# Performance work log

Measured on AMD Instinct MI355X. Metric: run time of the kernel, lower is better.

## Reference

```python
import jax, jax.numpy as jnp
import numpy as np
from jax import lax

D = 1024
DI = 2 * D          # mamba inner dim
NS = 16             # ssm state size
DTR = D // 16       # dt rank = 64
KC = 4              # conv kernel
E = 8               # experts
DFF = 2 * D         # expert hidden
TOPK = 2


def _ln(x, g, b):
    mu = x.mean(-1, keepdims=True)
    var = ((x - mu) ** 2).mean(-1, keepdims=True)
    return (x - mu) * lax.rsqrt(var + 1e-5) * g + b


def _silu(x):
    return x * jax.nn.sigmoid(x)


def setup_inputs() -> dict:
    key = jax.random.key(0)
    ks = jax.random.split(key, 20)
    s = 0.02
    inp = {
        "x": jax.random.normal(ks[0], (2, 2048, D), jnp.float32),
        # layernorms
        "ln_mamba_g": jnp.ones((D,), jnp.float32),
        "ln_mamba_b": jnp.zeros((D,), jnp.float32),
        "ln_moe_g": jnp.ones((D,), jnp.float32),
        "ln_moe_b": jnp.zeros((D,), jnp.float32),
        # mamba params
        "in_proj_w": jax.random.normal(ks[1], (2 * DI, D), jnp.float32) * s,
        "in_proj_b": jnp.zeros((2 * DI,), jnp.float32),
        "conv_w": jax.random.normal(ks[2], (DI, KC), jnp.float32) * s,
        "conv_b": jnp.zeros((DI,), jnp.float32),
        "x_proj_w": jax.random.normal(ks[3], (DTR + 2 * NS, DI), jnp.float32) * s,
        "dt_proj_w": jax.random.normal(ks[4], (DI, DTR), jnp.float32) * s,
        "dt_proj_b": jnp.full((DI,), -4.6, jnp.float32),  # softplus -> small dt
        "A_log": jnp.log(jnp.broadcast_to(jnp.arange(1, NS + 1, dtype=jnp.float32), (DI, NS))),
        "D_skip": jnp.ones((DI,), jnp.float32),
        "out_proj_w": jax.random.normal(ks[5], (D, DI), jnp.float32) * s,
        # moe params
        "router_w": jax.random.normal(ks[6], (E, D), jnp.float32) * s,
        "w1": jax.random.normal(ks[7], (E, DFF, D), jnp.float32) * s,
        "b1": jnp.zeros((E, DFF), jnp.float32),
        "w2": jax.random.normal(ks[8], (E, D, DFF), jnp.float32) * s,
        "b2": jnp.zeros((E, D), jnp.float32),
    }
    return inp


def _mamba(x, in_proj_w, in_proj_b, conv_w, conv_b, x_proj_w,
           dt_proj_w, dt_proj_b, A_log, D_skip, out_proj_w):
    Bz, T, _ = x.shape
    xz = x @ in_proj_w.T + in_proj_b            # [B,T,2*DI]
    xi, z = xz[..., :DI], xz[..., DI:]
    # causal depthwise conv, kernel 4
    xp = jnp.pad(xi, ((0, 0), (KC - 1, 0), (0, 0)))
    xc = conv_b + sum(conv_w[:, k] * xp[:, k:k + T, :] for k in range(KC))
    xc = _silu(xc)                              # [B,T,DI]
    proj = xc @ x_proj_w.T                      # [B,T,DTR+2*NS]
    dt_r = proj[..., :DTR]
    Bm = proj[..., DTR:DTR + NS]                # [B,T,NS]
    Cm = proj[..., DTR + NS:]                   # [B,T,NS]
    dt = jax.nn.softplus(dt_r @ dt_proj_w.T + dt_proj_b)  # [B,T,DI]
    A = -jnp.exp(A_log)                         # [DI,NS]

    def step(h, inp):
        xt, dtt, Bt, Ct = inp                   # [B,DI],[B,DI],[B,NS],[B,NS]
        dA = jnp.exp(dtt[:, :, None] * A)       # [B,DI,NS]
        h = dA * h + (dtt * xt)[:, :, None] * Bt[:, None, :]
        y = jnp.einsum('bdn,bn->bd', h, Ct)
        return h, y

    h0 = jnp.zeros((Bz, DI, NS), x.dtype)
    xs = (xc.transpose(1, 0, 2), dt.transpose(1, 0, 2),
          Bm.transpose(1, 0, 2), Cm.transpose(1, 0, 2))
    _, ys = lax.scan(step, h0, xs)              # [T,B,DI]
    y = ys.transpose(1, 0, 2) + xc * D_skip
    y = y * _silu(z)
    return y @ out_proj_w.T                     # [B,T,D]


def _moe(x, router_w, w1, b1, w2, b2):
    logits = x @ router_w.T                     # [B,T,E]
    probs = jax.nn.softmax(logits, axis=-1)
    topv, topi = lax.top_k(probs, TOPK)
    topv = topv / topv.sum(-1, keepdims=True)
    w = (jax.nn.one_hot(topi, E, dtype=x.dtype) * topv[..., None]).sum(-2)  # [B,T,E]
    out = jnp.zeros_like(x)
    for e in range(E):                          # fixed small expert loop
        h1 = _silu(x @ w1[e].T + b1[e])
        ye = h1 @ w2[e].T + b2[e]
        out = out + w[..., e:e + 1] * ye
    return out, {"router_probs": probs}


def reference(x, ln_mamba_g, ln_mamba_b, ln_moe_g, ln_moe_b,
              in_proj_w, in_proj_b, conv_w, conv_b, x_proj_w,
              dt_proj_w, dt_proj_b, A_log, D_skip, out_proj_w,
              router_w, w1, b1, w2, b2):
    h_norm = _ln(x, ln_mamba_g, ln_mamba_b)
    mamba_out = _mamba(h_norm, in_proj_w, in_proj_b, conv_w, conv_b, x_proj_w,
                       dt_proj_w, dt_proj_b, A_log, D_skip, out_proj_w)
    h = x + mamba_out
    h_moe_in = _ln(h, ln_moe_g, ln_moe_b)
    moe_delta, aux = _moe(h_moe_in, router_w, w1, b1, w2, b2)
    h = h + moe_delta
    return (h, aux["router_probs"])
```

## Files before the change

### kernel.cpp

```cpp
#include <hip/hip_runtime.h>
#include <hip/hip_bf16.h>
#include <math.h>

#define NTOK   4096
#define TSEQ   2048
#define DMODEL 1024
#define DINNER 2048
#define NSTATE 16
#define DTRANK 64
#define NEXP   8
#define DFF    2048
#define NCHUNK 32
#define CLEN   64

typedef __attribute__((ext_vector_type(8))) short short8;
typedef __attribute__((ext_vector_type(4))) float f32x4;

__device__ __forceinline__ float fast_rcp(float x){ return __builtin_amdgcn_rcpf(x); }
__device__ __forceinline__ float siluf(float x){ return x * fast_rcp(1.f + __expf(-x)); }

__device__ __forceinline__ unsigned short f2bf(float x){
  unsigned int u = __float_as_uint(x);
  unsigned int r = (u + 0x7FFFu + ((u >> 16) & 1u)) >> 16;
  return (unsigned short)r;
}

__device__ __forceinline__ void split4(float4 a, unsigned short* hi, unsigned short* lo){
  float av[4] = {a.x, a.y, a.z, a.w};
  #pragma unroll
  for (int j=0;j<4;j++){
    unsigned short hu = f2bf(av[j]);
    float hf = __uint_as_float((unsigned int)hu << 16);
    hi[j] = hu;
    lo[j] = f2bf(av[j] - hf);
  }
}

__global__ void zero_kernel(int* __restrict__ p){ p[threadIdx.x] = 0; }

__global__ __launch_bounds__(256) void split_kernel(
    const float* __restrict__ in, unsigned short* __restrict__ hi,
    unsigned short* __restrict__ lo, int n)
{
  int i = (blockIdx.x*256 + threadIdx.x)*4;
  if (i >= n) return;
  float4 v = *(const float4*)(in + i);
  unsigned short ht[4], lt[4];
  split4(v, ht, lt);
  uint2 hw, lw;
  hw.x = (unsigned)ht[0] | ((unsigned)ht[1]<<16);
  hw.y = (unsigned)ht[2] | ((unsigned)ht[3]<<16);
  lw.x = (unsigned)lt[0] | ((unsigned)lt[1]<<16);
  lw.y = (unsigned)lt[2] | ((unsigned)lt[3]<<16);
  *(uint2*)(hi+i) = hw;
  *(uint2*)(lo+i) = lw;
}

__global__ __launch_bounds__(256) void cvt_bf_kernel(
    const float* __restrict__ in, unsigned short* __restrict__ out, int n)
{
  int i = (blockIdx.x*256 + threadIdx.x)*8;
  if (i >= n) return;
  float4 a = *(const float4*)(in+i);
  float4 b = *(const float4*)(in+i+4);
  short8 v;
  v[0]=(short)f2bf(a.x); v[1]=(short)f2bf(a.y); v[2]=(short)f2bf(a.z); v[3]=(short)f2bf(a.w);
  v[4]=(short)f2bf(b.x); v[5]=(short)f2bf(b.y); v[6]=(short)f2bf(b.z); v[7]=(short)f2bf(b.w);
  *(short8*)(out+i) = v;
}

template<int EPI, int BM, bool PS>
__global__ __launch_bounds__(256) void gemm_big(
    const float* __restrict__ A,
    const unsigned short* __restrict__ Ahi, const unsigned short* __restrict__ Alo, int lda,
    const unsigned short* __restrict__ Whi, const unsigned short* __restrict__ Wlo, int ldw,
    int M, int N, int K,
    const float* __restrict__ bias,
    const float* __restrict__ resid, int ldr,
    float* __restrict__ out, int ldo)
{
  constexpr int RG  = BM/64;
  constexpr int TPR = 256/BM;
  constexpr int EA  = 32/TPR;
  const int tid = threadIdx.x;
  const int m0 = blockIdx.y * BM;
  const int n0 = blockIdx.x * 128;

  __shared__ __align__(16) unsigned short Ahs[BM*40];
  __shared__ __align__(16) unsigned short Als[BM*40];
  __shared__ __align__(16) unsigned short Whs[128*40];
  __shared__ __align__(16) unsigned short Wls[128*40];

  const int arow = tid / TPR;
  const int aseg = (tid % TPR) * EA;
  const int wrow = tid >> 1;
  const int wseg = (tid & 1) * 16;

  const float* Ap = PS ? nullptr : (A + (size_t)(m0 + arow)*lda + aseg);
  const unsigned short* Aph = PS ? (Ahi + (size_t)(m0 + arow)*lda + aseg) : nullptr;
  const unsigned short* Apl = PS ? (Alo + (size_t)(m0 + arow)*lda + aseg) : nullptr;
  const bool wok = (n0 + wrow) < N;
  const unsigned short* Whp = Whi + (size_t)(n0 + wrow)*ldw + wseg;
  const unsigned short* Wlp = Wlo + (size_t)(n0 + wrow)*ldw + wseg;

  const int lane = tid & 63;
  const int wv   = tid >> 6;
  const int qd   = lane >> 4;
  const int mr   = lane & 15;

  f32x4 acc[RG][8];
  #pragma unroll
  for (int rg=0; rg<RG; rg++)
    #pragma unroll
    for (int ct=0; ct<8; ct++) acc[rg][ct] = (f32x4){0.f,0.f,0.f,0.f};

  const unsigned short* ardh = &Ahs[(wv*(16*RG) + mr)*40 + qd*8];
  const unsigned short* ardl = &Als[(wv*(16*RG) + mr)*40 + qd*8];
  const unsigned short* brdh = &Whs[mr*40 + qd*8];
  const unsigned short* brdl = &Wls[mr*40 + qd*8];

  const short8 z8 = {0,0,0,0,0,0,0,0};

  for (int kt = 0; kt < K; kt += 32){
    short8 ah[EA/8], al[EA/8];
    if (PS){
      #pragma unroll
      for (int h=0; h<EA/8; h++){
        ah[h] = *(const short8*)(Aph + kt + h*8);
        al[h] = *(const short8*)(Apl + kt + h*8);
      }
    } else {
      #pragma unroll
      for (int q=0; q<EA/4; q++){
        float4 f = *(const float4*)(Ap + kt + q*4);
        unsigned short ht[4], lt[4];
        split4(f, ht, lt);
        #pragma unroll
        for (int j=0;j<4;j++){
          ah[(q*4+j)/8][(q*4+j)&7] = (short)ht[j];
          al[(q*4+j)/8][(q*4+j)&7] = (short)lt[j];
        }
      }
    }
    short8 wh0 = wok ? *(const short8*)(Whp + kt)     : z8;
    short8 wh1 = wok ? *(const short8*)(Whp + kt + 8) : z8;
    short8 wl0 = wok ? *(const short8*)(Wlp + kt)     : z8;
    short8 wl1 = wok ? *(const short8*)(Wlp + kt + 8) : z8;
    __syncthreads();
    #pragma unroll
    for (int h=0; h<EA/8; h++){
      *(short8*)&Ahs[arow*40 + aseg + h*8] = ah[h];
      *(short8*)&Als[arow*40 + aseg + h*8] = al[h];
    }
    *(short8*)&Whs[wrow*40 + wseg]     = wh0;
    *(short8*)&Whs[wrow*40 + wseg + 8] = wh1;
    *(short8*)&Wls[wrow*40 + wseg]     = wl0;
    *(short8*)&Wls[wrow*40 + wseg + 8] = wl1;
    __syncthreads();
    #pragma unroll
    for (int rg=0; rg<RG; rg++){
      short8 af = *(const short8*)(ardh + rg*16*40);
      short8 alf= *(const short8*)(ardl + rg*16*40);
      #pragma unroll
      for (int ct=0; ct<8; ct++){
        short8 bh = *(const short8*)(brdh + ct*16*40);
        short8 bl = *(const short8*)(brdl + ct*16*40);
        f32x4 t = acc[rg][ct];
        t = __builtin_amdgcn_mfma_f32_16x16x32_bf16(af, bh, t, 0,0,0);
        t = __builtin_amdgcn_mfma_f32_16x16x32_bf16(alf, bh, t, 0,0,0);
        t = __builtin_amdgcn_mfma_f32_16x16x32_bf16(af, bl, t, 0,0,0);
        acc[rg][ct] = t;
      }
    }
  }

  #pragma unroll
  for (int rg=0; rg<RG; rg++){
    #pragma unroll
    for (int ct=0; ct<8; ct++){
      int colg = n0 + ct*16 + mr;
      if (colg >= N) continue;
      float bias_v = (EPI==0 || EPI==2) ? bias[colg] : 0.f;
      #pragma unroll
      for (int r=0;r<4;r++){
        int rowg = m0 + wv*(16*RG) + rg*16 + qd*4 + r;
        float v = acc[rg][ct][r];
        if (EPI == 0){ v += bias_v; }
        else if (EPI == 2){ v += bias_v; v = (v > 20.f) ? v : log1pf(expf(v)); }
        else if (EPI == 3){ v += resid[(size_t)rowg*ldr + colg]; }
        out[(size_t)rowg*ldo + colg] = v;
      }
    }
  }
}

__global__ __launch_bounds__(256) void ln_split_kernel(
    const float* __restrict__ x, const float* __restrict__ g, const float* __restrict__ b,
    unsigned short* __restrict__ hi, unsigned short* __restrict__ lo)
{
  int tok = blockIdx.x;
  int tid = threadIdx.x;
  const float* row = x + (size_t)tok * DMODEL;
  float v[4];
  float s = 0.f, sq = 0.f;
  #pragma unroll
  for (int j=0;j<4;j++){
    v[j] = row[j*256 + tid];
    s += v[j]; sq += v[j]*v[j];
  }
  #pragma unroll
  for (int o=1;o<64;o<<=1){ s += __shfl_xor(s,o,64); sq += __shfl_xor(sq,o,64); }
  __shared__ float ss[4], ssq[4];
  int wid = tid >> 6, lane = tid & 63;
  if (lane == 0){ ss[wid]=s; ssq[wid]=sq; }
  __syncthreads();
  s  = ss[0]+ss[1]+ss[2]+ss[3];
  sq = ssq[0]+ssq[1]+ssq[2]+ssq[3];
  float mu = s * (1.f/DMODEL);
  float var = sq * (1.f/DMODEL) - mu*mu;
  float rs = rsqrtf(var + 1e-5f);
  #pragma unroll
  for (int j=0;j<4;j++){
    int d = j*256 + tid;
    float o = (v[j]-mu)*rs*g[d] + b[d];
    unsigned short hu = f2bf(o);
    float hf = __uint_as_float((unsigned int)hu << 16);
    hi[(size_t)tok*DMODEL + d] = hu;
    lo[(size_t)tok*DMODEL + d] = f2bf(o - hf);
  }
}

__global__ __launch_bounds__(256) void ln2_kernel(
    const float* __restrict__ x, const float* __restrict__ g, const float* __restrict__ b,
    float* __restrict__ out, unsigned short* __restrict__ outb)
{
  int tok = blockIdx.x;
  int tid = threadIdx.x;
  const float* row = x + (size_t)tok * DMODEL;
  float v[4];
  float s = 0.f, sq = 0.f;
  #pragma unroll
  for (int j=0;j<4;j++){
    v[j] = row[j*256 + tid];
    s += v[j]; sq += v[j]*v[j];
  }
  #pragma unroll
  for (int o=1;o<64;o<<=1){ s += __shfl_xor(s,o,64); sq += __shfl_xor(sq,o,64); }
  __shared__ float ss[4], ssq[4];
  int wid = tid >> 6, lane = tid & 63;
  if (lane == 0){ ss[wid]=s; ssq[wid]=sq; }
  __syncthreads();
  s  = ss[0]+ss[1]+ss[2]+ss[3];
  sq = ssq[0]+ssq[1]+ssq[2]+ssq[3];
  float mu = s * (1.f/DMODEL);
  float var = sq * (1.f/DMODEL) - mu*mu;
  float rs = rsqrtf(var + 1e-5f);
  #pragma unroll
  for (int j=0;j<4;j++){
    int d = j*256 + tid;
    float o = (v[j]-mu)*rs*g[d] + b[d];
    out[(size_t)tok*DMODEL + d] = o;
    outb[(size_t)tok*DMODEL + d] = f2bf(o);
  }
}

__global__ __launch_bounds__(256) void conv_kernel(
    const float* __restrict__ xz, const float* __restrict__ cw,
    const float* __restrict__ cb, float* __restrict__ xc)
{
  int i = blockIdx.x*256 + threadIdx.x;
  int tok = i >> 11;
  int ch  = i & 2047;
  int t   = tok & (TSEQ-1);
  int b   = tok >> 11;
  float acc = cb[ch];
  #pragma unroll
  for (int k=0;k<4;k++){
    int tt = t + k - 3;
    if (tt >= 0)
      acc = fmaf(cw[ch*4 + k], xz[(size_t)((b<<11)+tt)*4096 + ch], acc);
  }
  xc[i] = siluf(acc);
}

__global__ __launch_bounds__(256) void scan_partial(
    const float* __restrict__ xz, const float* __restrict__ xc,
    const float* __restrict__ proj, const float* __restrict__ A_log,
    float* __restrict__ P, float* __restrict__ Q)
{
  int tid = threadIdx.x;
  int ch  = blockIdx.x*256 + tid;
  int c   = blockIdx.y;
  int b   = blockIdx.z;
  float A[16];
  #pragma unroll
  for (int n=0;n<16;n++) A[n] = -expf(A_log[ch*NSTATE + n]);
  float h[16];
  #pragma unroll
  for (int n=0;n<16;n++) h[n] = 0.f;
  float sdt = 0.f;
  int tok0 = (b<<11) + c*CLEN;
  float dtv = xz[(size_t)tok0*4096 + ch];
  float xt  = xc[(size_t)tok0*2048 + ch];
  for (int i=0;i<CLEN;i++){
    int tn = tok0 + ((i+1 < CLEN) ? i+1 : i);
    float dtv_n = xz[(size_t)tn*4096 + ch];
    float xt_n  = xc[(size_t)tn*2048 + ch];
    const float4* pB = (const float4*)(proj + (size_t)(tok0+i)*96 + 64);
    float Bv[16];
    *(float4*)&Bv[0]  = pB[0];
    *(float4*)&Bv[4]  = pB[1];
    *(float4*)&Bv[8]  = pB[2];
    *(float4*)&Bv[12] = pB[3];
    float dxt = dtv*xt;
    sdt += dtv;
    #pragma unroll
    for (int n=0;n<16;n++){
      float dA = __expf(dtv*A[n]);
      h[n] = fmaf(dA, h[n], dxt*Bv[n]);
    }
    dtv = dtv_n; xt = xt_n;
  }
  size_t base = ((((size_t)(b*NCHUNK + c))<<11 | ch)<<4);
  #pragma unroll
  for (int n=0;n<16;n++){
    P[base+n] = __expf(A[n]*sdt);
    Q[base+n] = h[n];
  }
}

__global__ __launch_bounds__(256) void scan_combine(
    const float* __restrict__ Q, float* PH)
{
  int g = blockIdx.x*256 + threadIdx.x;
  int n = g & 15, ch = (g>>4) & 2047, b = g>>15;
  float hs = 0.f;
  for (int c=0;c<NCHUNK;c++){
    size_t idx = ((((size_t)(b*NCHUNK + c))<<11 | ch)<<4) | n;
    float pv = PH[idx];
    float qv = Q[idx];
    PH[idx] = hs;
    hs = fmaf(pv, hs, qv);
  }
}

__global__ __launch_bounds__(256) void scan_final(
    const float* __restrict__ xz, float* __restrict__ xc,
    const float* __restrict__ proj, const float* __restrict__ A_log,
    const float* __restrict__ Dskip, const float* __restrict__ Hs)
{
  int tid = threadIdx.x;
  int ch  = blockIdx.x*256 + tid;
  int c   = blockIdx.y;
  int b   = blockIdx.z;
  float A[16];
  #pragma unroll
  for (int n=0;n<16;n++) A[n] = -expf(A_log[ch*NSTATE + n]);
  float Dv = Dskip[ch];
  size_t base = ((((size_t)(b*NCHUNK + c))<<11 | ch)<<4);
  float h[16];
  #pragma unroll
  for (int n=0;n<16;n++) h[n] = Hs[base+n];
  int tok0 = (b<<11) + c*CLEN;
  float dtv = xz[(size_t)tok0*4096 + ch];
  float xt  = xc[(size_t)tok0*2048 + ch];
  float zv  = xz[(size_t)tok0*4096 + 2048 + ch];
  for (int i=0;i<CLEN;i++){
    int tn = tok0 + ((i+1 < CLEN) ? i+1 : i);
    float dtv_n = xz[(size_t)tn*4096 + ch];
    float xt_n  = xc[(size_t)tn*2048 + ch];
    float zv_n  = xz[(size_t)tn*4096 + 2048 + ch];
    const float4* pB = (const float4*)(proj + (size_t)(tok0+i)*96 + 64);
    float Bv[16], Cv[16];
    *(float4*)&Bv[0]  = pB[0];
    *(float4*)&Bv[4]  = pB[1];
    *(float4*)&Bv[8]  = pB[2];
    *(float4*)&Bv[12] = pB[3];
    *(float4*)&Cv[0]  = pB[4];
    *(float4*)&Cv[4]  = pB[5];
    *(float4*)&Cv[8]  = pB[6];
    *(float4*)&Cv[12] = pB[7];
    float dxt = dtv*xt;
    float y = xt*Dv;
    #pragma unroll
    for (int n=0;n<16;n++){
      float dA = __expf(dtv*A[n]);
      h[n] = fmaf(dA, h[n], dxt*Bv[n]);
      y = fmaf(h[n], Cv[n], y);
    }
    xc[(size_t)(tok0+i)*2048 + ch] = y * siluf(zv);
    dtv = dtv_n; xt = xt_n; zv = zv_n;
  }
}

__global__ __launch_bounds__(256) void router_kernel(
    const float* __restrict__ hmoe, const float* __restrict__ rw,
    float* __restrict__ probs_out, int* __restrict__ cnt,
    int* __restrict__ tok_e0, int* __restrict__ tok_e1,
    float* __restrict__ tok_w0, float* __restrict__ tok_w1)
{
  int tok = blockIdx.x;
  int tid = threadIdx.x;
  int e = tid >> 5, l = tid & 31;
  float s = 0.f;
  const float* row = hmoe + (size_t)tok*DMODEL;
  const float* wr  = rw + (size_t)e*DMODEL;
  for (int d=l; d<DMODEL; d+=32) s = fmaf(row[d], wr[d], s);
  #pragma unroll
  for (int o=1;o<32;o<<=1) s += __shfl_xor(s,o,64);
  __shared__ float lg[8];
  if (l==0) lg[e]=s;
  __syncthreads();
  if (tid==0){
    float mx = lg[0];
    for (int k=1;k<8;k++) mx = fmaxf(mx, lg[k]);
    float pe[8]; float den=0.f;
    for (int k=0;k<8;k++){ pe[k]=expf(lg[k]-mx); den+=pe[k]; }
    float inv = 1.f/den;
    for (int k=0;k<8;k++) probs_out[tok*8+k] = pe[k]*inv;
    int i0=0;
    for (int k=1;k<8;k++) if (pe[k] > pe[i0]) i0=k;
    int i1 = (i0==0)?1:0;
    for (int k=0;k<8;k++) if (k!=i0 && pe[k] > pe[i1]) i1=k;
    float v0=pe[i0], v1=pe[i1], sw=v0+v1;
    tok_e0[tok]=i0; tok_e1[tok]=i1;
    tok_w0[tok]=v0/sw; tok_w1[tok]=v1/sw;
    atomicAdd(&cnt[i0],1); atomicAdd(&cnt[i1],1);
  }
}

__global__ void prefix_kernel(const int* cnt, int* off, int* fill){
  if (threadIdx.x==0){
    int s=0;
    for (int e=0;e<NEXP;e++){ off[e]=s; s+=cnt[e]; fill[e]=0; }
  }
}

__global__ __launch_bounds__(256) void fill_kernel(
    const int* tok_e0, const int* tok_e1, const float* tok_w0, const float* tok_w1,
    const int* off, int* fill, int* slot_tok, float* slot_w)
{
  int tok = blockIdx.x*256 + threadIdx.x;
  int e0=tok_e0[tok], e1=tok_e1[tok];
  int p0 = atomicAdd(&fill[e0],1); int s0 = off[e0]+p0;
  slot_tok[s0]=tok; slot_w[s0]=tok_w0[tok];
  int p1 = atomicAdd(&fill[e1],1); int s1 = off[e1]+p1;
  slot_tok[s1]=tok; slot_w[s1]=tok_w1[tok];
}

__global__ __launch_bounds__(256) void moe_gemm1(
    const unsigned short* __restrict__ hnb, const unsigned short* __restrict__ w1b,
    const float* __restrict__ b1,
    const int* __restrict__ cnt, const int* __restrict__ off,
    const int* __restrict__ slot_tok, unsigned short* __restrict__ H1)
{
  int e = blockIdx.z;
  int c = cnt[e];
  int r0 = blockIdx.y*128;
  if (r0 >= c) return;
  int base = off[e];
  int tid = threadIdx.x;
  __shared__ int toks[128];
  if (tid < 128) toks[tid] = (r0 + tid < c) ? slot_tok[base + r0 + tid] : -1;
  __shared__ __align__(16) unsigned short As[128*40];
  __shared__ __align__(16) unsigned short Ws[128*40];
  __syncthreads();

  const int n0   = blockIdx.x*128;
  const int srow = tid >> 1;
  const int sseg = (tid & 1) * 16;
  const int tok  = toks[srow];
  const bool aok = (tok >= 0);
  const unsigned short* Ap = hnb + (size_t)(aok ? tok : 0)*DMODEL + sseg;
  const unsigned short* Wp = w1b + (size_t)e*DFF*DMODEL + (size_t)(n0+srow)*DMODEL + sseg;

  const int lane = tid & 63;
  const int wv   = tid >> 6;
  const int qd   = lane >> 4;
  const int mr   = lane & 15;

  f32x4 acc[2][8];
  #pragma unroll
  for (int rg=0; rg<2; rg++)
    #pragma unroll
    for (int ct=0; ct<8; ct++) acc[rg][ct] = (f32x4){0.f,0.f,0.f,0.f};

  const unsigned short* ard = &As[(wv*32 + mr)*40 + qd*8];
  const unsigned short* brd = &Ws[mr*40 + qd*8];
  const short8 z8 = {0,0,0,0,0,0,0,0};

  for (int kt = 0; kt < DMODEL; kt += 32){
    short8 a0 = aok ? *(const short8*)(Ap + kt)     : z8;
    short8 a1 = aok ? *(const short8*)(Ap + kt + 8) : z8;
    short8 w0 = *(const short8*)(Wp + kt);
    short8 w1v= *(const short8*)(Wp + kt + 8);
    __syncthreads();
    *(short8*)&As[srow*40 + sseg]     = a0;
    *(short8*)&As[srow*40 + sseg + 8] = a1;
    *(short8*)&Ws[srow*40 + sseg]     = w0;
    *(short8*)&Ws[srow*40 + sseg + 8] = w1v;
    __syncthreads();
    #pragma unroll
    for (int rg=0; rg<2; rg++){
      short8 af = *(const short8*)(ard + rg*16*40);
      #pragma unroll
      for (int ct=0; ct<8; ct++){
        short8 bf = *(const short8*)(brd + ct*16*40);
        acc[rg][ct] = __builtin_amdgcn_mfma_f32_16x16x32_bf16(af, bf, acc[rg][ct], 0,0,0);
      }
    }
  }

  #pragma unroll
  for (int rg=0; rg<2; rg++){
    #pragma unroll
    for (int ct=0; ct<8; ct++){
      int colg = n0 + ct*16 + mr;
      float bias = b1[(size_t)e*DFF + colg];
      #pragma unroll
      for (int r=0;r<4;r++){
        int sl = wv*32 + rg*16 + qd*4 + r;
        if (toks[sl] < 0) continue;
        float v = acc[rg][ct][r] + bias;
        H1[(size_t)(base + r0 + sl)*DFF + colg] = f2bf(siluf(v));
      }
    }
  }
}

__global__ __launch_bounds__(256) void moe_gemm2(
    const unsigned short* __restrict__ H1, const unsigned short* __restrict__ w2b,
    const float* __restrict__ b2,
    const int* __restrict__ cnt, const int* __restrict__ off,
    const int* __restrict__ slot_tok, const float* __restrict__ slot_w,
    float* __restrict__ hres)
{
  int e = blockIdx.z;
  int c = cnt[e];
  int r0 = blockIdx.y*128;
  if (r0 >= c) return;
  int base = off[e];
  int tid = threadIdx.x;
  __shared__ int toks[128];
  __shared__ float wts[128];
  if (tid < 128){
    int r = r0 + tid;
    toks[tid] = (r<c) ? slot_tok[base+r] : -1;
    wts[tid]  = (r<c) ? slot_w[base+r] : 0.f;
  }
  __shared__ __align__(16) unsigned short As[128*40];
  __shared__ __align__(16) unsigned short Ws[128*40];
  __syncthreads();

  const int n0   = blockIdx.x*128;
  const int srow = tid >> 1;
  const int sseg = (tid & 1) * 16;
  const bool aok = (toks[srow] >= 0);
  const unsigned short* Ap = H1 + (size_t)(base + r0 + (aok ? srow : 0))*DFF + sseg;
  const unsigned short* Wp = w2b + (size_t)e*DMODEL*DFF + (size_t)(n0+srow)*DFF + sseg;

  const int lane = tid & 63;
  const int wv   = tid >> 6;
  const int qd   = lane >> 4;
  const int mr   = lane & 15;

  f32x4 acc[2][8];
  #pragma unroll
  for (int rg=0; rg<2; rg++)
    #pragma unroll
    for (int ct=0; ct<8; ct++) acc[rg][ct] = (f32x4){0.f,0.f,0.f,0.f};

  const unsigned short* ard = &As[(wv*32 + mr)*40 + qd*8];
  const unsigned short* brd = &Ws[mr*40 + qd*8];
  const short8 z8 = {0,0,0,0,0,0,0,0};

  for (int kt = 0; kt < DFF; kt += 32){
    short8 a0 = aok ? *(const short8*)(Ap + kt)     : z8;
    short8 a1 = aok ? *(const short8*)(Ap + kt + 8) : z8;
    short8 w0 = *(const short8*)(Wp + kt);
    short8 w1v= *(const short8*)(Wp + kt + 8);
    __syncthreads();
    *(short8*)&As[srow*40 + sseg]     = a0;
    *(short8*)&As[srow*40 + sseg + 8] = a1;
    *(short8*)&Ws[srow*40 + sseg]     = w0;
    *(short8*)&Ws[srow*40 + sseg + 8] = w1v;
    __syncthreads();
    #pragma unroll
    for (int rg=0; rg<2; rg++){
      short8 af = *(const short8*)(ard + rg*16*40);
      #pragma unroll
      for (int ct=0; ct<8; ct++){
        short8 bf = *(const short8*)(brd + ct*16*40);
        acc[rg][ct] = __builtin_amdgcn_mfma_f32_16x16x32_bf16(af, bf, acc[rg][ct], 0,0,0);
      }
    }
  }

  #pragma unroll
  for (int rg=0; rg<2; rg++){
    #pragma unroll
    for (int ct=0; ct<8; ct++){
      int colg = n0 + ct*16 + mr;
      float bias = b2[(size_t)e*DMODEL + colg];
      #pragma unroll
      for (int r=0;r<4;r++){
        int sl = wv*32 + rg*16 + qd*4 + r;
        int t = toks[sl];
        if (t < 0) continue;
        float v = acc[rg][ct][r] + bias;
        atomicAdd(&hres[(size_t)t*DMODEL + colg], wts[sl]*v);
      }
    }
  }
}

__global__ __launch_bounds__(256) void final_kernel(const float* __restrict__ hres,
                                                    float* __restrict__ out)
{
  int i = blockIdx.x*256 + threadIdx.x;
  out[i] = hres[i];
}

extern "C" void kernel_launch(void* const* d_in, const int* in_sizes, int n_in,
                              void* d_out, int out_size, void* d_ws, size_t ws_size,
                              hipStream_t stream)
{
  const float* x         = (const float*)d_in[0];
  const float* ln_m_g    = (const float*)d_in[1];
  const float* ln_m_b    = (const float*)d_in[2];
  const float* ln_e_g    = (const float*)d_in[3];
  const float* ln_e_b    = (const float*)d_in[4];
  const float* in_proj_w = (const float*)d_in[5];
  const float* in_proj_b = (const float*)d_in[6];
  const float* conv_w    = (const float*)d_in[7];
  const float* conv_b    = (const float*)d_in[8];
  const float* x_proj_w  = (const float*)d_in[9];
  const float* dt_proj_w = (const float*)d_in[10];
  const float* dt_proj_b = (const float*)d_in[11];
  const float* A_log     = (const float*)d_in[12];
  const float* D_skip    = (const float*)d_in[13];
  const float* out_proj_w= (const float*)d_in[14];
  const float* router_w  = (const float*)d_in[15];
  const float* w1        = (const float*)d_in[16];
  const float* b1        = (const float*)d_in[17];
  const float* w2        = (const float*)d_in[18];
  const float* b2        = (const float*)d_in[19];

  char* ws = (char*)d_ws;
  float* xz   = (float*)(ws + 0);
  float* xc   = (float*)(ws + 67108864ull);
  float* proj = (float*)(ws + 100663296ull);
  char*  misc = ws + 102236160ull;
  float* hres = (float*)(ws + 0);
  unsigned short* H1    = (unsigned short*)(ws + 16777216ull);
  unsigned short* hn_bf = (unsigned short*)(ws + 50331648ull);
  unsigned short* wmoe  = (unsigned short*)(ws + 67108864ull);

  unsigned short* hn_hi = (unsigned short*)d_out;
  unsigned short* hn_lo = hn_hi + 4194304;
  float* hn   = (float*)d_out;
  float* Pbuf = (float*)d_out;
  float* Qbuf = (float*)d_out + (2u<<20);

  unsigned short* Wi_hi = (unsigned short*)(ws + 67108864ull);
  unsigned short* Wi_lo = Wi_hi + 4194304;
  unsigned short* Wo_hi = (unsigned short*)(ws + 33554432ull);
  unsigned short* Wo_lo = Wo_hi + 2097152;
  unsigned short* Wx_hi = (unsigned short*)d_out;
  unsigned short* Wx_lo = Wx_hi + 196608;
  unsigned short* Wd_hi = Wx_lo + 196608;
  unsigned short* Wd_lo = Wd_hi + 131072;

  int*   cnt      = (int*)(misc);
  int*   fill     = (int*)(misc + 64);
  int*   offp     = (int*)(misc + 128);
  int*   tok_e0   = (int*)(misc + 1024);
  int*   tok_e1   = (int*)(misc + 1024 + 16384);
  float* tok_w0   = (float*)(misc + 1024 + 32768);
  float* tok_w1   = (float*)(misc + 1024 + 49152);
  int*   slot_tok = (int*)(misc + 1024 + 65536);
  float* slot_w   = (float*)(misc + 1024 + 98304);
  float* out_h    = (float*)d_out;
  float* probs_out= (float*)d_out + 4194304;

  zero_kernel<<<1, 64, 0, stream>>>(cnt);

  split_kernel<<<4096, 256, 0, stream>>>(in_proj_w, Wi_hi, Wi_lo, 4194304);
  ln_split_kernel<<<NTOK, 256, 0, stream>>>(x, ln_m_g, ln_m_b, hn_hi, hn_lo);
  gemm_big<0,128,true><<<dim3(32, 32), 256, 0, stream>>>(
      nullptr, hn_hi, hn_lo, DMODEL, Wi_hi, Wi_lo, DMODEL, NTOK, 4096, DMODEL,
      in_proj_b, nullptr, 0, xz, 4096);
  split_kernel<<<192, 256, 0, stream>>>(x_proj_w, Wx_hi, Wx_lo, 196608);
  split_kernel<<<128, 256, 0, stream>>>(dt_proj_w, Wd_hi, Wd_lo, 131072);
  conv_kernel<<<NTOK*DINNER/256, 256, 0, stream>>>(xz, conv_w, conv_b, xc);
  gemm_big<1,64,false><<<dim3(1, 64), 256, 0, stream>>>(
      xc, nullptr, nullptr, DINNER, Wx_hi, Wx_lo, DINNER, NTOK, 96, DINNER,
      nullptr, nullptr, 0, proj, 96);
  gemm_big<2,128,false><<<dim3(16, 32), 256, 0, stream>>>(
      proj, nullptr, nullptr, 96, Wd_hi, Wd_lo, DTRANK, NTOK, DINNER, DTRANK,
      dt_proj_b, nullptr, 0, xz, 4096);
  scan_partial<<<dim3(DINNER/256, NCHUNK, 2), 256, 0, stream>>>(
      xz, xc, proj, A_log, Pbuf, Qbuf);
  scan_combine<<<256, 256, 0, stream>>>(Qbuf, Pbuf);
  scan_final<<<dim3(DINNER/256, NCHUNK, 2), 256, 0, stream>>>(
      xz, xc, proj, A_log, D_skip, Pbuf);
  split_kernel<<<2048, 256, 0, stream>>>(out_proj_w, Wo_hi, Wo_lo, 2097152);
  gemm_big<3,128,false><<<dim3(8, 32), 256, 0, stream>>>(
      xc, nullptr, nullptr, DINNER, Wo_hi, Wo_lo, DINNER, NTOK, DMODEL, DINNER,
      nullptr, x, DMODEL, hres, DMODEL);

  ln2_kernel<<<NTOK, 256, 0, stream>>>(hres, ln_e_g, ln_e_b, hn, hn_bf);
  router_kernel<<<NTOK, 256, 0, stream>>>(hn, router_w, probs_out, cnt,
                                          tok_e0, tok_e1, tok_w0, tok_w1);
  prefix_kernel<<<1, 64, 0, stream>>>(cnt, offp, fill);
  fill_kernel<<<NTOK/256, 256, 0, stream>>>(tok_e0, tok_e1, tok_w0, tok_w1,
                                            offp, fill, slot_tok, slot_w);
  cvt_bf_kernel<<<8192, 256, 0, stream>>>(w1, wmoe, NEXP*DFF*DMODEL);
  moe_gemm1<<<dim3(DFF/128, 32, NEXP), 256, 0, stream>>>(
      hn_bf, wmoe, b1, cnt, offp, slot_tok, H1);
  cvt_bf_kernel<<<8192, 256, 0, stream>>>(w2, wmoe, NEXP*DMODEL*DFF);
  moe_gemm2<<<dim3(DMODEL/128, 32, NEXP), 256, 0, stream>>>(
      H1, wmoe, b2, cnt, offp, slot_tok, slot_w, hres);

  final_kernel<<<NTOK*DMODEL/256, 256, 0, stream>>>(hres, out_h);
}
```

Measured before the change: 1.056 ms.

## Add split-K and configurable N-tile to gemm, widen in_proj tile, drop final copy

The generic GEMM gains a templated N-tile width and a split-K mode that writes per-slice partial outputs. The narrow x_proj GEMM (N=96) is split four ways along K and the out_proj GEMM two ways, with small reduction kernels summing the partials (the out_proj one also adds the residual). The in_proj GEMM switches to a 256-wide N tile. The MoE accumulates directly into the output buffer, which removes the final copy kernel. The goal is more parallelism for the small-grid GEMMs and less redundant A-tile traffic, paid for by extra partial-sum memory traffic, extra launches and higher register pressure from the wider tile.

```diff
diff --git a/kernel.cpp b/kernel.cpp
--- a/kernel.cpp
+++ b/kernel.cpp
@@ -69,50 +69,54 @@
   *(short8*)(out+i) = v;
 }
 
-template<int EPI, int BM, bool PS>
+template<int EPI, int BM, bool PS, int CT, bool SK>
 __global__ __launch_bounds__(256) void gemm_big(
     const float* __restrict__ A,
     const unsigned short* __restrict__ Ahi, const unsigned short* __restrict__ Alo, int lda,
     const unsigned short* __restrict__ Whi, const unsigned short* __restrict__ Wlo, int ldw,
     int M, int N, int K,
     const float* __restrict__ bias,
-    const float* __restrict__ resid, int ldr,
     float* __restrict__ out, int ldo)
 {
+  constexpr int BN  = CT*16;
   constexpr int RG  = BM/64;
   constexpr int TPR = 256/BM;
   constexpr int EA  = 32/TPR;
+  constexpr int TPW = 256/BN;
+  constexpr int EW  = 32/TPW;
   const int tid = threadIdx.x;
   const int m0 = blockIdx.y * BM;
-  const int n0 = blockIdx.x * 128;
+  const int n0 = blockIdx.x * BN;
+  const int koff = SK ? blockIdx.z * K : 0;
+  float* outp = out + (SK ? (size_t)blockIdx.z * M * ldo : 0);
 
   __shared__ __align__(16) unsigned short Ahs[BM*40];
   __shared__ __align__(16) unsigned short Als[BM*40];
-  __shared__ __align__(16) unsigned short Whs[128*40];
-  __shared__ __align__(16) unsigned short Wls[128*40];
+  __shared__ __align__(16) unsigned short Whs[BN*40];
+  __shared__ __align__(16) unsigned short Wls[BN*40];
 
   const int arow = tid / TPR;
   const int aseg = (tid % TPR) * EA;
-  const int wrow = tid >> 1;
-  const int wseg = (tid & 1) * 16;
-
-  const float* Ap = PS ? nullptr : (A + (size_t)(m0 + arow)*lda + aseg);
-  const unsigned short* Aph = PS ? (Ahi + (size_t)(m0 + arow)*lda + aseg) : nullptr;
-  const unsigned short* Apl = PS ? (Alo + (size_t)(m0 + arow)*lda + aseg) : nullptr;
+  const int wrow = tid / TPW;
+  const int wseg = (tid % TPW) * EW;
+
+  const float* Ap = PS ? nullptr : (A + (size_t)(m0 + arow)*lda + aseg + koff);
+  const unsigned short* Aph = PS ? (Ahi + (size_t)(m0 + arow)*lda + aseg + koff) : nullptr;
+  const unsigned short* Apl = PS ? (Alo + (size_t)(m0 + arow)*lda + aseg + koff) : nullptr;
   const bool wok = (n0 + wrow) < N;
-  const unsigned short* Whp = Whi + (size_t)(n0 + wrow)*ldw + wseg;
-  const unsigned short* Wlp = Wlo + (size_t)(n0 + wrow)*ldw + wseg;
+  const unsigned short* Whp = Whi + (size_t)(n0 + wrow)*ldw + wseg + koff;
+  const unsigned short* Wlp = Wlo + (size_t)(n0 + wrow)*ldw + wseg + koff;
 
   const int lane = tid & 63;
   const int wv   = tid >> 6;
   const int qd   = lane >> 4;
   const int mr   = lane & 15;
 
-  f32x4 acc[RG][8];
+  f32x4 acc[RG][CT];
   #pragma unroll
   for (int rg=0; rg<RG; rg++)
     #pragma unroll
-    for (int ct=0; ct<8; ct++) acc[rg][ct] = (f32x4){0.f,0.f,0.f,0.f};
+    for (int ct=0; ct<CT; ct++) acc[rg][ct] = (f32x4){0.f,0.f,0.f,0.f};
 
   const unsigned short* ardh = &Ahs[(wv*(16*RG) + mr)*40 + qd*8];
   const unsigned short* ardl = &Als[(wv*(16*RG) + mr)*40 + qd*8];
@@ -142,27 +146,30 @@
         }
       }
     }
-    short8 wh0 = wok ? *(const short8*)(Whp + kt)     : z8;
-    short8 wh1 = wok ? *(const short8*)(Whp + kt + 8) : z8;
-    short8 wl0 = wok ? *(const short8*)(Wlp + kt)     : z8;
-    short8 wl1 = wok ? *(const short8*)(Wlp + kt + 8) : z8;
+    short8 wh[EW/8], wl[EW/8];
+    #pragma unroll
+    for (int h=0; h<EW/8; h++){
+      wh[h] = wok ? *(const short8*)(Whp + kt + h*8) : z8;
+      wl[h] = wok ? *(const short8*)(Wlp + kt + h*8) : z8;
+    }
     __syncthreads();
     #pragma unroll
     for (int h=0; h<EA/8; h++){
       *(short8*)&Ahs[arow*40 + aseg + h*8] = ah[h];
       *(short8*)&Als[arow*40 + aseg + h*8] = al[h];
     }
-    *(short8*)&Whs[wrow*40 + wseg]     = wh0;
-    *(short8*)&Whs[wrow*40 + wseg + 8] = wh1;
-    *(short8*)&Wls[wrow*40 + wseg]     = wl0;
-    *(short8*)&Wls[wrow*40 + wseg + 8] = wl1;
+    #pragma unroll
+    for (int h=0; h<EW/8; h++){
+      *(short8*)&Whs[wrow*40 + wseg + h*8] = wh[h];
+      *(short8*)&Wls[wrow*40 + wseg + h*8] = wl[h];
+    }
     __syncthreads();
     #pragma unroll
     for (int rg=0; rg<RG; rg++){
       short8 af = *(const short8*)(ardh + rg*16*40);
       short8 alf= *(const short8*)(ardl + rg*16*40);
       #pragma unroll
-      for (int ct=0; ct<8; ct++){
+      for (int ct=0; ct<CT; ct++){
         short8 bh = *(const short8*)(brdh + ct*16*40);
         short8 bl = *(const short8*)(brdl + ct*16*40);
         f32x4 t = acc[rg][ct];
@@ -177,7 +184,7 @@
   #pragma unroll
   for (int rg=0; rg<RG; rg++){
     #pragma unroll
-    for (int ct=0; ct<8; ct++){
+    for (int ct=0; ct<CT; ct++){
       int colg = n0 + ct*16 + mr;
       if (colg >= N) continue;
       float bias_v = (EPI==0 || EPI==2) ? bias[colg] : 0.f;
@@ -187,11 +194,41 @@
         float v = acc[rg][ct][r];
         if (EPI == 0){ v += bias_v; }
         else if (EPI == 2){ v += bias_v; v = (v > 20.f) ? v : log1pf(expf(v)); }
-        else if (EPI == 3){ v += resid[(size_t)rowg*ldr + colg]; }
-        out[(size_t)rowg*ldo + colg] = v;
+        outp[(size_t)rowg*ldo + colg] = v;
       }
     }
   }
+}
+
+__global__ __launch_bounds__(256) void reduce4_kernel(
+    const float* __restrict__ pp, float* __restrict__ out, int n)
+{
+  int i = (blockIdx.x*256 + threadIdx.x)*4;
+  if (i >= n) return;
+  float4 a = *(const float4*)(pp + i);
+  float4 b = *(const float4*)(pp + n + i);
+  float4 c = *(const float4*)(pp + 2*(size_t)n + i);
+  float4 d = *(const float4*)(pp + 3*(size_t)n + i);
+  float4 o;
+  o.x = (a.x+b.x)+(c.x+d.x);
+  o.y = (a.y+b.y)+(c.y+d.y);
+  o.z = (a.z+b.z)+(c.z+d.z);
+  o.w = (a.w+b.w)+(c.w+d.w);
+  *(float4*)(out + i) = o;
+}
+
+__global__ __launch_bounds__(256) void reduce2r_kernel(
+    const float* __restrict__ p0, const float* __restrict__ p1,
+    const float* __restrict__ r, float* __restrict__ out, int n)
+{
+  int i = (blockIdx.x*256 + threadIdx.x)*4;
+  if (i >= n) return;
+  float4 a = *(const float4*)(p0 + i);
+  float4 b = *(const float4*)(p1 + i);
+  float4 c = *(const float4*)(r + i);
+  float4 o;
+  o.x = a.x+b.x+c.x; o.y = a.y+b.y+c.y; o.z = a.z+b.z+c.z; o.w = a.w+b.w+c.w;
+  *(float4*)(out + i) = o;
 }
 
 __global__ __launch_bounds__(256) void ln_split_kernel(
@@ -614,13 +651,6 @@
   }
 }
 
-__global__ __launch_bounds__(256) void final_kernel(const float* __restrict__ hres,
-                                                    float* __restrict__ out)
-{
-  int i = blockIdx.x*256 + threadIdx.x;
-  out[i] = hres[i];
-}
-
 extern "C" void kernel_launch(void* const* d_in, const int* in_sizes, int n_in,
                               void* d_out, int out_size, void* d_ws, size_t ws_size,
                               hipStream_t stream)
@@ -651,20 +681,21 @@
   float* xc   = (float*)(ws + 67108864ull);
   float* proj = (float*)(ws + 100663296ull);
   char*  misc = ws + 102236160ull;
-  float* hres = (float*)(ws + 0);
+  float* hn   = (float*)(ws + 0);
+  float* pout = (float*)(ws + 16777216ull);
   unsigned short* H1    = (unsigned short*)(ws + 16777216ull);
   unsigned short* hn_bf = (unsigned short*)(ws + 50331648ull);
   unsigned short* wmoe  = (unsigned short*)(ws + 67108864ull);
 
   unsigned short* hn_hi = (unsigned short*)d_out;
   unsigned short* hn_lo = hn_hi + 4194304;
-  float* hn   = (float*)d_out;
   float* Pbuf = (float*)d_out;
   float* Qbuf = (float*)d_out + (2u<<20);
+  float* ppx  = (float*)((char*)d_out + 2097152ull);
 
   unsigned short* Wi_hi = (unsigned short*)(ws + 67108864ull);
   unsigned short* Wi_lo = Wi_hi + 4194304;
-  unsigned short* Wo_hi = (unsigned short*)(ws + 33554432ull);
+  unsigned short* Wo_hi = (unsigned short*)Qbuf;
   unsigned short* Wo_lo = Wo_hi + 2097152;
   unsigned short* Wx_hi = (unsigned short*)d_out;
   unsigned short* Wx_lo = Wx_hi + 196608;
@@ -687,29 +718,32 @@
 
   split_kernel<<<4096, 256, 0, stream>>>(in_proj_w, Wi_hi, Wi_lo, 4194304);
   ln_split_kernel<<<NTOK, 256, 0, stream>>>(x, ln_m_g, ln_m_b, hn_hi, hn_lo);
-  gemm_big<0,128,true><<<dim3(32, 32), 256, 0, stream>>>(
+  gemm_big<0,128,true,16,false><<<dim3(16, 32), 256, 0, stream>>>(
       nullptr, hn_hi, hn_lo, DMODEL, Wi_hi, Wi_lo, DMODEL, NTOK, 4096, DMODEL,
-      in_proj_b, nullptr, 0, xz, 4096);
+      in_proj_b, xz, 4096);
   split_kernel<<<192, 256, 0, stream>>>(x_proj_w, Wx_hi, Wx_lo, 196608);
   split_kernel<<<128, 256, 0, stream>>>(dt_proj_w, Wd_hi, Wd_lo, 131072);
   conv_kernel<<<NTOK*DINNER/256, 256, 0, stream>>>(xz, conv_w, conv_b, xc);
-  gemm_big<1,64,false><<<dim3(1, 64), 256, 0, stream>>>(
-      xc, nullptr, nullptr, DINNER, Wx_hi, Wx_lo, DINNER, NTOK, 96, DINNER,
-      nullptr, nullptr, 0, proj, 96);
-  gemm_big<2,128,false><<<dim3(16, 32), 256, 0, stream>>>(
+  gemm_big<1,64,false,8,true><<<dim3(1, 64, 4), 256, 0, stream>>>(
+      xc, nullptr, nullptr, DINNER, Wx_hi, Wx_lo, DINNER, NTOK, 96, 512,
+      nullptr, ppx, 96);
+  reduce4_kernel<<<384, 256, 0, stream>>>(ppx, proj, NTOK*96);
+  gemm_big<2,128,false,8,false><<<dim3(16, 32), 256, 0, stream>>>(
       proj, nullptr, nullptr, 96, Wd_hi, Wd_lo, DTRANK, NTOK, DINNER, DTRANK,
-      dt_proj_b, nullptr, 0, xz, 4096);
+      dt_proj_b, xz, 4096);
   scan_partial<<<dim3(DINNER/256, NCHUNK, 2), 256, 0, stream>>>(
       xz, xc, proj, A_log, Pbuf, Qbuf);
   scan_combine<<<256, 256, 0, stream>>>(Qbuf, Pbuf);
   scan_final<<<dim3(DINNER/256, NCHUNK, 2), 256, 0, stream>>>(
       xz, xc, proj, A_log, D_skip, Pbuf);
   split_kernel<<<2048, 256, 0, stream>>>(out_proj_w, Wo_hi, Wo_lo, 2097152);
-  gemm_big<3,128,false><<<dim3(8, 32), 256, 0, stream>>>(
-      xc, nullptr, nullptr, DINNER, Wo_hi, Wo_lo, DINNER, NTOK, DMODEL, DINNER,
-      nullptr, x, DMODEL, hres, DMODEL);
-
-  ln2_kernel<<<NTOK, 256, 0, stream>>>(hres, ln_e_g, ln_e_b, hn, hn_bf);
+  gemm_big<1,128,false,8,true><<<dim3(8, 32, 2), 256, 0, stream>>>(
+      xc, nullptr, nullptr, DINNER, Wo_hi, Wo_lo, DINNER, NTOK, DMODEL, 1024,
+      nullptr, pout, DMODEL);
+  reduce2r_kernel<<<4096, 256, 0, stream>>>(pout, pout + 4194304, x, out_h,
+                                            NTOK*DMODEL);
+
+  ln2_kernel<<<NTOK, 256, 0, stream>>>(out_h, ln_e_g, ln_e_b, hn, hn_bf);
   router_kernel<<<NTOK, 256, 0, stream>>>(hn, router_w, probs_out, cnt,
                                           tok_e0, tok_e1, tok_w0, tok_w1);
   prefix_kernel<<<1, 64, 0, stream>>>(cnt, offp, fill);
@@ -720,7 +754,5 @@
       hn_bf, wmoe, b1, cnt, offp, slot_tok, H1);
   cvt_bf_kernel<<<8192, 256, 0, stream>>>(w2, wmoe, NEXP*DMODEL*DFF);
   moe_gemm2<<<dim3(DMODEL/128, 32, NEXP), 256, 0, stream>>>(
-      H1, wmoe, b2, cnt, offp, slot_tok, slot_w, hres);
-
-  final_kernel<<<NTOK*DMODEL/256, 256, 0, stream>>>(hres, out_h);
-}
+      H1, wmoe, b2, cnt, offp, slot_tok, slot_w, out_h);
+}
```

New measurement: 1.095 ms. 1.04x slower.
